# Kernel tuning notes

Hardware: AMD Instinct MI355X
Metric: run time of the kernel (lower is better)

Reference implementation:

```python
import jax, jax.numpy as jnp
import numpy as np

SEQ_LEN = 512
DIM = 256
HEADS = 8
DIM_HEAD = 32
INNER = HEADS * DIM_HEAD
BATCH = 1
LN_EPS = 1e-5


def setup_inputs() -> dict:
    key = jax.random.key(0)
    ks = jax.random.split(key, 6)
    # kaiming_uniform_(a=sqrt(5)) on [L, in, out] -> bound = 1/sqrt(fan_in) with fan_in = in_dim*out_dim? 
    # torch computes fan_in from dims [1:] => fan_in = in_dim (dim of -2) * ... in practice bound ~ sqrt(1/fan_in);
    # exact init distribution is irrelevant for correctness testing, use uniform(+-1/sqrt(DIM)).
    s = 1.0 / np.sqrt(DIM)
    so = 1.0 / np.sqrt(INNER)
    return {
        "x": jax.random.normal(ks[0], (BATCH, SEQ_LEN, DIM), jnp.float32),
        "Wq": jax.random.uniform(ks[1], (SEQ_LEN, DIM, INNER), jnp.float32, -s, s),
        "Wk": jax.random.uniform(ks[2], (SEQ_LEN, DIM, INNER), jnp.float32, -s, s),
        "Wv": jax.random.uniform(ks[3], (SEQ_LEN, DIM, INNER), jnp.float32, -s, s),
        "gamma": jnp.ones((DIM,), jnp.float32),
        "beta": jnp.zeros((DIM,), jnp.float32),
        "Wo": jax.random.uniform(ks[4], (INNER, DIM), jnp.float32, -so, so),
        "bo": jnp.zeros((DIM,), jnp.float32),
    }


def reference(x, Wq, Wk, Wv, gamma, beta, Wo, bo):
    b, n, dim = x.shape
    h, dh = HEADS, DIM_HEAD
    # LayerNorm
    mu = jnp.mean(x, axis=-1, keepdims=True)
    var = jnp.mean((x - mu) ** 2, axis=-1, keepdims=True)
    xn = (x - mu) / jnp.sqrt(var + LN_EPS) * gamma + beta
    # Per-relative-index projections: pd[b, r, m, e] = xn[b, m] @ W[r]
    qd = jnp.einsum('bmc,rce->brme', xn, Wq)
    kd = jnp.einsum('bmc,rce->brme', xn, Wk)
    vd = jnp.einsum('bmc,rce->brme', xn, Wv)
    i = jnp.arange(n)
    # to_q / to_v index map: max(0, i - j); to_k (after rearrange swap) uses min(0, m - n) + n - 1
    rq = jnp.maximum(0, i[:, None] - i[None, :])          # [n(query), m(key)]
    rk = jnp.minimum(0, i[None, :] - i[:, None]) + n - 1  # [n, m]
    # q[b,n,m,e] = qd[b, rq[n,m], m]; k[b,n,m,e] = kd[b, rk[n,m], n]; v like q
    q_full = qd[:, rq, i[None, :], :].reshape(b, n, n, h, dh)
    k_full = kd[:, rk, i[:, None], :].reshape(b, n, n, h, dh)
    v_full = vd[:, rq, i[None, :], :].reshape(b, n, n, h, dh)
    scale = dh ** -0.5
    dots = jnp.einsum('bnmhd,bnmhd->bhnm', q_full, k_full) * scale
    causal = i[:, None] >= i[None, :]  # tril
    dots = jnp.where(causal[None, None], dots, -jnp.inf)
    attn = jax.nn.softmax(dots, axis=-1)
    out = jnp.einsum('bhnm,bnmhd->bnhd', attn, v_full).reshape(b, n, h * dh)
    return out @ Wo + bo
```

## Files before the change

kernel.cpp:

```cpp
#include <hip/hip_runtime.h>
#include <hip/hip_bf16.h>

typedef unsigned short u16;
typedef unsigned int   u32;
typedef __bf16 bf16x8 __attribute__((ext_vector_type(8)));
typedef float  f32x4  __attribute__((ext_vector_type(4)));
typedef u32    u32x4  __attribute__((ext_vector_type(4)));
typedef u32    u32x2  __attribute__((ext_vector_type(2)));

#define TRI_TOTAL 131328

__device__ __forceinline__ float b2f(u16 u) {
    return __builtin_bit_cast(float, ((u32)u) << 16);
}
__device__ __forceinline__ u16 f2b(float f) {
    u32 u = __builtin_bit_cast(u32, f);
    return (u16)((u + 0x7fffu + ((u >> 16) & 1u)) >> 16);
}

__global__ void __launch_bounds__(256) ln_kernel(const float* __restrict__ x,
                                                 const float* __restrict__ g,
                                                 const float* __restrict__ b,
                                                 u16* __restrict__ xn) {
    int n = blockIdx.x, t = threadIdx.x;
    float v = x[n * 256 + t];
    __shared__ float red[4];
    float s = v;
    #pragma unroll
    for (int o = 32; o >= 1; o >>= 1) s += __shfl_xor(s, o);
    if ((t & 63) == 0) red[t >> 6] = s;
    __syncthreads();
    float mu = (red[0] + red[1] + red[2] + red[3]) * (1.0f / 256.0f);
    float d = v - mu;
    __syncthreads();
    float s2 = d * d;
    #pragma unroll
    for (int o = 32; o >= 1; o >>= 1) s2 += __shfl_xor(s2, o);
    if ((t & 63) == 0) red[t >> 6] = s2;
    __syncthreads();
    float var = (red[0] + red[1] + red[2] + red[3]) * (1.0f / 256.0f);
    float y = d * rsqrtf(var + 1e-5f) * g[t] + b[t];
    xn[n * 256 + t] = f2b(y);
}

__global__ void __launch_bounds__(256) proj_kernel(
        const u16* __restrict__ xn,
        const float* __restrict__ Wq, const float* __restrict__ Wk,
        const float* __restrict__ Wv,
        u16* __restrict__ Qa, u16* __restrict__ Ka, u16* __restrict__ Va) {
    __shared__ u16 Wl[64 * 256];
    __shared__ u16 Al[64 * 256];

    int bid = blockIdx.x;
    int which = bid >> 11;
    int rr = bid & 2047;
    int r  = (which == 1) ? (511 - (rr >> 2)) : (rr >> 2);
    int cs = rr & 3;
    const float* W = (which == 0) ? Wq : ((which == 1) ? Wk : Wv);
    u16* Out       = (which == 0) ? Qa : ((which == 1) ? Ka : Va);
    int rows  = (which == 1) ? (r + 1) : (512 - r);
    int pbase = (which == 1) ? (511 - r) : 0;
    int nbase = (which == 1) ? (511 - r) : r;

    int t = threadIdx.x;
    int c0 = cs * 64;

    int srow   = t >> 5;
    int slot16 = (t & 31) * 16;
    char* adp = (char*)Al + srow * 512 + (slot16 ^ (srow << 4));
    u32x4 ar0, ar1, ar2, ar3, ar4, ar5, ar6, ar7;

#define A_LOAD(M0) do {                                                       \
    int gg;                                                                   \
    gg = pbase + (M0) +  0 + srow; if (gg > 511) gg = 511;                    \
    ar0 = *(const u32x4*)((const char*)xn + (size_t)gg * 512 + slot16);       \
    gg = pbase + (M0) +  8 + srow; if (gg > 511) gg = 511;                    \
    ar1 = *(const u32x4*)((const char*)xn + (size_t)gg * 512 + slot16);       \
    gg = pbase + (M0) + 16 + srow; if (gg > 511) gg = 511;                    \
    ar2 = *(const u32x4*)((const char*)xn + (size_t)gg * 512 + slot16);       \
    gg = pbase + (M0) + 24 + srow; if (gg > 511) gg = 511;                    \
    ar3 = *(const u32x4*)((const char*)xn + (size_t)gg * 512 + slot16);       \
    gg = pbase + (M0) + 32 + srow; if (gg > 511) gg = 511;                    \
    ar4 = *(const u32x4*)((const char*)xn + (size_t)gg * 512 + slot16);       \
    gg = pbase + (M0) + 40 + srow; if (gg > 511) gg = 511;                    \
    ar5 = *(const u32x4*)((const char*)xn + (size_t)gg * 512 + slot16);       \
    gg = pbase + (M0) + 48 + srow; if (gg > 511) gg = 511;                    \
    ar6 = *(const u32x4*)((const char*)xn + (size_t)gg * 512 + slot16);       \
    gg = pbase + (M0) + 56 + srow; if (gg > 511) gg = 511;                    \
    ar7 = *(const u32x4*)((const char*)xn + (size_t)gg * 512 + slot16);       \
} while (0)

#define A_WRITE() do {                                                        \
    *(u32x4*)(adp + 0 * 4096) = ar0;                                          \
    *(u32x4*)(adp + 1 * 4096) = ar1;                                          \
    *(u32x4*)(adp + 2 * 4096) = ar2;                                          \
    *(u32x4*)(adp + 3 * 4096) = ar3;                                          \
    *(u32x4*)(adp + 4 * 4096) = ar4;                                          \
    *(u32x4*)(adp + 5 * 4096) = ar5;                                          \
    *(u32x4*)(adp + 6 * 4096) = ar6;                                          \
    *(u32x4*)(adp + 7 * 4096) = ar7;                                          \
} while (0)

    {
        int c4 = (t & 15) * 4;
        int kq = t >> 4;
        const float* wp = W + ((size_t)r << 16) + c0 + c4 + (size_t)(kq * 4) * 256;
        f32x4 w00 = *(const f32x4*)(wp + 0 * 256);
        f32x4 w01 = *(const f32x4*)(wp + 1 * 256);
        f32x4 w02 = *(const f32x4*)(wp + 2 * 256);
        f32x4 w03 = *(const f32x4*)(wp + 3 * 256);
        f32x4 w10 = *(const f32x4*)(wp + 16384 + 0 * 256);
        f32x4 w11 = *(const f32x4*)(wp + 16384 + 1 * 256);
        f32x4 w12 = *(const f32x4*)(wp + 16384 + 2 * 256);
        f32x4 w13 = *(const f32x4*)(wp + 16384 + 3 * 256);
        f32x4 w20 = *(const f32x4*)(wp + 32768 + 0 * 256);
        f32x4 w21 = *(const f32x4*)(wp + 32768 + 1 * 256);
        f32x4 w22 = *(const f32x4*)(wp + 32768 + 2 * 256);
        f32x4 w23 = *(const f32x4*)(wp + 32768 + 3 * 256);
        f32x4 w30 = *(const f32x4*)(wp + 49152 + 0 * 256);
        f32x4 w31 = *(const f32x4*)(wp + 49152 + 1 * 256);
        f32x4 w32 = *(const f32x4*)(wp + 49152 + 2 * 256);
        f32x4 w33 = *(const f32x4*)(wp + 49152 + 3 * 256);
        A_LOAD(0);
#define WLW(IT, VA, VB, VC, VD) {                                             \
        int kbase = kq * 4 + (IT) * 64;                                       \
        _Pragma("unroll")                                                     \
        for (int i = 0; i < 4; ++i) {                                         \
            int col = c4 + i;                                                 \
            u32 lo = (u32)f2b(VA[i]) | ((u32)f2b(VB[i]) << 16);               \
            u32 hi = (u32)f2b(VC[i]) | ((u32)f2b(VD[i]) << 16);               \
            u32x2 pr; pr[0] = lo; pr[1] = hi;                                 \
            *(u32x2*)((char*)Wl + col * 512 +                                 \
                      ((kbase * 2) ^ ((col & 31) << 4))) = pr;                \
        }                                                                     \
    }
        WLW(0, w00, w01, w02, w03)
        WLW(1, w10, w11, w12, w13)
        WLW(2, w20, w21, w22, w23)
        WLW(3, w30, w31, w32, w33)
#undef WLW
    }
    __syncthreads();

    int wv  = t >> 6;
    int L   = t & 63;
    int l15 = L & 15, l4 = L >> 4;
    int rbase = wv * 16;
    const char* wb = (const char*)Wl;
    const char* al_row = (const char*)Al + (rbase + l15) * 512;
    int amask = ((rbase + l15) & 7) << 4;
    int cA = l15, cB = 16 + l15, cC = 32 + l15, cD = 48 + l15;
    int swA = (cA & 31) << 4, swB = (cB & 31) << 4;
    int swC = (cC & 31) << 4, swD = (cD & 31) << 4;

    for (int m0 = 0; m0 < rows; m0 += 64) {
        A_WRITE();
        __syncthreads();
        if (m0 + 64 < rows) A_LOAD(m0 + 64);

        f32x4 acc0 = {}, acc1 = {}, acc2 = {}, acc3 = {};
#define KS(ks) {                                                              \
        int kb = (ks) * 64 + l4 * 16;                                         \
        bf16x8 a  = *(const bf16x8*)(al_row + (kb ^ amask));                  \
        bf16x8 b0 = *(const bf16x8*)(wb + cA * 512 + (kb ^ swA));             \
        bf16x8 b1 = *(const bf16x8*)(wb + cB * 512 + (kb ^ swB));             \
        bf16x8 b2 = *(const bf16x8*)(wb + cC * 512 + (kb ^ swC));             \
        bf16x8 b3 = *(const bf16x8*)(wb + cD * 512 + (kb ^ swD));             \
        acc0 = __builtin_amdgcn_mfma_f32_16x16x32_bf16(a, b0, acc0, 0, 0, 0); \
        acc1 = __builtin_amdgcn_mfma_f32_16x16x32_bf16(a, b1, acc1, 0, 0, 0); \
        acc2 = __builtin_amdgcn_mfma_f32_16x16x32_bf16(a, b2, acc2, 0, 0, 0); \
        acc3 = __builtin_amdgcn_mfma_f32_16x16x32_bf16(a, b3, acc3, 0, 0, 0); \
    }
        KS(0) KS(1) KS(2) KS(3) KS(4) KS(5) KS(6) KS(7)
#undef KS

        #pragma unroll
        for (int j = 0; j < 4; ++j) {
            int ml = m0 + rbase + l4 * 4 + j;
            if (ml < rows) {
                int nout = nbase + ml;
                size_t prow = (size_t)(nout * (nout + 1) / 2) + (size_t)ml;
                u16* op = Out + prow * 256 + c0 + l15;
                op[0]  = f2b(acc0[j]);
                op[16] = f2b(acc1[j]);
                op[32] = f2b(acc2[j]);
                op[48] = f2b(acc3[j]);
            }
        }
        __syncthreads();
    }
#undef A_LOAD
#undef A_WRITE
}

__global__ void __launch_bounds__(256) attn_kernel(const u16* __restrict__ Qa,
                                                   const u16* __restrict__ Ka,
                                                   const u16* __restrict__ Va,
                                                   float* __restrict__ ao) {
    int n = blockIdx.x, t = threadIdx.x;
    __shared__ float pbuf[512 * 9];
    __shared__ float linv[8];
    int band = n + 1;
    size_t rb = (size_t)(n * (n + 1) / 2);

    int h = t & 7, mi = t >> 3;
    for (int m0 = 0; m0 < band; m0 += 32) {
        int m = m0 + mi;
        float d = -1e30f;
        if (m < band) {
            const char* qp = (const char*)Qa + (rb + m) * 512 + h * 64;
            const char* kp = (const char*)Ka + (rb + m) * 512 + h * 64;
            float acc = 0.f;
            #pragma unroll
            for (int cch = 0; cch < 4; ++cch) {
                u32x4 qv = *reinterpret_cast<const u32x4*>(qp + cch * 16);
                u32x4 kv = *reinterpret_cast<const u32x4*>(kp + cch * 16);
                #pragma unroll
                for (int i = 0; i < 4; ++i) {
                    float ql = __builtin_bit_cast(float, qv[i] << 16);
                    float qh = __builtin_bit_cast(float, qv[i] & 0xffff0000u);
                    float kl = __builtin_bit_cast(float, kv[i] << 16);
                    float kh = __builtin_bit_cast(float, kv[i] & 0xffff0000u);
                    acc += ql * kl + qh * kh;
                }
            }
            d = acc * 0.17677669529663687f;
        }
        pbuf[m * 9 + h] = d;
    }
    __syncthreads();

    int wv = t >> 6, L = t & 63;
    for (int s = 0; s < 2; ++s) {
        int hh = wv + s * 4;
        float mx = -1e30f;
        for (int m = L; m < band; m += 64) mx = fmaxf(mx, pbuf[m * 9 + hh]);
        #pragma unroll
        for (int o = 32; o >= 1; o >>= 1) mx = fmaxf(mx, __shfl_xor(mx, o));
        float sum = 0.f;
        for (int m = L; m < band; m += 64) {
            float p = __expf(pbuf[m * 9 + hh] - mx);
            pbuf[m * 9 + hh] = p;
            sum += p;
        }
        #pragma unroll
        for (int o = 32; o >= 1; o >>= 1) sum += __shfl_xor(sum, o);
        if (L == 0) linv[hh] = 1.0f / sum;
    }
    __syncthreads();

    int h2 = t >> 5;
    const char* vp = (const char*)Va + rb * 512 + (size_t)t * 2;
    const float* pb = pbuf + h2;
    float a0 = 0, a1 = 0, a2 = 0, a3 = 0;
    int m = 0;
    for (; m + 4 <= band; m += 4) {
        a0 += pb[(m + 0) * 9] * b2f(*(const u16*)(vp + (size_t)(m + 0) * 512));
        a1 += pb[(m + 1) * 9] * b2f(*(const u16*)(vp + (size_t)(m + 1) * 512));
        a2 += pb[(m + 2) * 9] * b2f(*(const u16*)(vp + (size_t)(m + 2) * 512));
        a3 += pb[(m + 3) * 9] * b2f(*(const u16*)(vp + (size_t)(m + 3) * 512));
    }
    for (; m < band; ++m)
        a0 += pb[m * 9] * b2f(*(const u16*)(vp + (size_t)m * 512));
    ao[n * 256 + t] = ((a0 + a1) + (a2 + a3)) * linv[h2];
}

__global__ void __launch_bounds__(256) outproj_kernel(const float* __restrict__ ao,
                                                      const float* __restrict__ Wo,
                                                      const float* __restrict__ bo,
                                                      float* __restrict__ out) {
    int n = blockIdx.x, e = threadIdx.x;
    const float* a = ao + n * 256;
    float c0 = bo[e], c1 = 0, c2 = 0, c3 = 0;
    for (int c = 0; c < 256; c += 4) {
        c0 += a[c + 0] * Wo[(c + 0) * 256 + e];
        c1 += a[c + 1] * Wo[(c + 1) * 256 + e];
        c2 += a[c + 2] * Wo[(c + 2) * 256 + e];
        c3 += a[c + 3] * Wo[(c + 3) * 256 + e];
    }
    out[n * 256 + e] = (c0 + c1) + (c2 + c3);
}

extern "C" void kernel_launch(void* const* d_in, const int* in_sizes, int n_in,
                              void* d_out, int out_size, void* d_ws, size_t ws_size,
                              hipStream_t stream) {
    const float* x     = (const float*)d_in[0];
    const float* Wq    = (const float*)d_in[1];
    const float* Wk    = (const float*)d_in[2];
    const float* Wv    = (const float*)d_in[3];
    const float* gamma = (const float*)d_in[4];
    const float* beta  = (const float*)d_in[5];
    const float* Wo    = (const float*)d_in[6];
    const float* bo    = (const float*)d_in[7];
    float* out = (float*)d_out;

    char* ws = (char*)d_ws;
    u16* xn = (u16*)ws;
    size_t off = (size_t)512 * 256 * 2;
    u16* Qa = (u16*)(ws + off); off += (size_t)TRI_TOTAL * 256 * 2;
    u16* Ka = (u16*)(ws + off); off += (size_t)TRI_TOTAL * 256 * 2;
    u16* Va = (u16*)(ws + off); off += (size_t)TRI_TOTAL * 256 * 2;
    float* ao = (float*)(ws + off);

    ln_kernel<<<512, 256, 0, stream>>>(x, gamma, beta, xn);
    proj_kernel<<<6144, 256, 0, stream>>>(xn, Wq, Wk, Wv, Qa, Ka, Va);
    attn_kernel<<<512, 256, 0, stream>>>(Qa, Ka, Va, ao);
    outproj_kernel<<<512, 256, 0, stream>>>(ao, Wo, bo, out);
}
```

Measured before the change: 274.0 us.

## Split projection tile across eight waves with column-group partitioning

Doubles the projection kernel block to 512 threads. The 64x64 output tile is now split into 4 row groups and 2 column groups, so each wave computes 16x32 instead of 16x64. Weight and activation staging loads are spread over twice as many threads, with fewer registers held per thread, and the LDS swizzle for weight columns changes to a new XOR pattern. The aim is more memory-level parallelism and latency hiding on the bandwidth-heavy weight reads, at the cost of per-wave fragment reuse and larger blocks that may limit how many blocks fit per CU.

```diff
diff --git a/kernel.cpp b/kernel.cpp
--- a/kernel.cpp
+++ b/kernel.cpp
@@ -16,6 +16,9 @@
 __device__ __forceinline__ u16 f2b(float f) {
     u32 u = __builtin_bit_cast(u32, f);
     return (u16)((u + 0x7fffu + ((u >> 16) & 1u)) >> 16);
+}
+__device__ __forceinline__ int pcol(int col) {
+    return (((col & 7) ^ ((col >> 3) & 7)) << 4);
 }
 
 __global__ void __launch_bounds__(256) ln_kernel(const float* __restrict__ x,
@@ -43,7 +46,7 @@
     xn[n * 256 + t] = f2b(y);
 }
 
-__global__ void __launch_bounds__(256) proj_kernel(
+__global__ void __launch_bounds__(512) proj_kernel(
         const u16* __restrict__ xn,
         const float* __restrict__ Wq, const float* __restrict__ Wk,
         const float* __restrict__ Wv,
@@ -67,109 +70,82 @@
 
     int srow   = t >> 5;
     int slot16 = (t & 31) * 16;
-    char* adp = (char*)Al + srow * 512 + (slot16 ^ (srow << 4));
-    u32x4 ar0, ar1, ar2, ar3, ar4, ar5, ar6, ar7;
+    char* adp = (char*)Al + srow * 512 + (slot16 ^ ((srow & 7) << 4));
+    u32x4 ar0, ar1, ar2, ar3;
 
 #define A_LOAD(M0) do {                                                       \
     int gg;                                                                   \
     gg = pbase + (M0) +  0 + srow; if (gg > 511) gg = 511;                    \
     ar0 = *(const u32x4*)((const char*)xn + (size_t)gg * 512 + slot16);       \
-    gg = pbase + (M0) +  8 + srow; if (gg > 511) gg = 511;                    \
+    gg = pbase + (M0) + 16 + srow; if (gg > 511) gg = 511;                    \
     ar1 = *(const u32x4*)((const char*)xn + (size_t)gg * 512 + slot16);       \
-    gg = pbase + (M0) + 16 + srow; if (gg > 511) gg = 511;                    \
+    gg = pbase + (M0) + 32 + srow; if (gg > 511) gg = 511;                    \
     ar2 = *(const u32x4*)((const char*)xn + (size_t)gg * 512 + slot16);       \
-    gg = pbase + (M0) + 24 + srow; if (gg > 511) gg = 511;                    \
+    gg = pbase + (M0) + 48 + srow; if (gg > 511) gg = 511;                    \
     ar3 = *(const u32x4*)((const char*)xn + (size_t)gg * 512 + slot16);       \
-    gg = pbase + (M0) + 32 + srow; if (gg > 511) gg = 511;                    \
-    ar4 = *(const u32x4*)((const char*)xn + (size_t)gg * 512 + slot16);       \
-    gg = pbase + (M0) + 40 + srow; if (gg > 511) gg = 511;                    \
-    ar5 = *(const u32x4*)((const char*)xn + (size_t)gg * 512 + slot16);       \
-    gg = pbase + (M0) + 48 + srow; if (gg > 511) gg = 511;                    \
-    ar6 = *(const u32x4*)((const char*)xn + (size_t)gg * 512 + slot16);       \
-    gg = pbase + (M0) + 56 + srow; if (gg > 511) gg = 511;                    \
-    ar7 = *(const u32x4*)((const char*)xn + (size_t)gg * 512 + slot16);       \
 } while (0)
 
 #define A_WRITE() do {                                                        \
-    *(u32x4*)(adp + 0 * 4096) = ar0;                                          \
-    *(u32x4*)(adp + 1 * 4096) = ar1;                                          \
-    *(u32x4*)(adp + 2 * 4096) = ar2;                                          \
-    *(u32x4*)(adp + 3 * 4096) = ar3;                                          \
-    *(u32x4*)(adp + 4 * 4096) = ar4;                                          \
-    *(u32x4*)(adp + 5 * 4096) = ar5;                                          \
-    *(u32x4*)(adp + 6 * 4096) = ar6;                                          \
-    *(u32x4*)(adp + 7 * 4096) = ar7;                                          \
+    *(u32x4*)(adp + 0 * 8192) = ar0;                                          \
+    *(u32x4*)(adp + 1 * 8192) = ar1;                                          \
+    *(u32x4*)(adp + 2 * 8192) = ar2;                                          \
+    *(u32x4*)(adp + 3 * 8192) = ar3;                                          \
 } while (0)
 
     {
         int c4 = (t & 15) * 4;
         int kq = t >> 4;
         const float* wp = W + ((size_t)r << 16) + c0 + c4 + (size_t)(kq * 4) * 256;
-        f32x4 w00 = *(const f32x4*)(wp + 0 * 256);
-        f32x4 w01 = *(const f32x4*)(wp + 1 * 256);
-        f32x4 w02 = *(const f32x4*)(wp + 2 * 256);
-        f32x4 w03 = *(const f32x4*)(wp + 3 * 256);
-        f32x4 w10 = *(const f32x4*)(wp + 16384 + 0 * 256);
-        f32x4 w11 = *(const f32x4*)(wp + 16384 + 1 * 256);
-        f32x4 w12 = *(const f32x4*)(wp + 16384 + 2 * 256);
-        f32x4 w13 = *(const f32x4*)(wp + 16384 + 3 * 256);
-        f32x4 w20 = *(const f32x4*)(wp + 32768 + 0 * 256);
-        f32x4 w21 = *(const f32x4*)(wp + 32768 + 1 * 256);
-        f32x4 w22 = *(const f32x4*)(wp + 32768 + 2 * 256);
-        f32x4 w23 = *(const f32x4*)(wp + 32768 + 3 * 256);
-        f32x4 w30 = *(const f32x4*)(wp + 49152 + 0 * 256);
-        f32x4 w31 = *(const f32x4*)(wp + 49152 + 1 * 256);
-        f32x4 w32 = *(const f32x4*)(wp + 49152 + 2 * 256);
-        f32x4 w33 = *(const f32x4*)(wp + 49152 + 3 * 256);
+        f32x4 w00 = *(const f32x4*)(wp + 0);
+        f32x4 w01 = *(const f32x4*)(wp + 256);
+        f32x4 w02 = *(const f32x4*)(wp + 512);
+        f32x4 w03 = *(const f32x4*)(wp + 768);
+        f32x4 w10 = *(const f32x4*)(wp + 32768 + 0);
+        f32x4 w11 = *(const f32x4*)(wp + 32768 + 256);
+        f32x4 w12 = *(const f32x4*)(wp + 32768 + 512);
+        f32x4 w13 = *(const f32x4*)(wp + 32768 + 768);
         A_LOAD(0);
 #define WLW(IT, VA, VB, VC, VD) {                                             \
-        int kbase = kq * 4 + (IT) * 64;                                       \
+        int kbase2 = (kq * 4 + (IT) * 128) * 2;                               \
         _Pragma("unroll")                                                     \
         for (int i = 0; i < 4; ++i) {                                         \
             int col = c4 + i;                                                 \
             u32 lo = (u32)f2b(VA[i]) | ((u32)f2b(VB[i]) << 16);               \
             u32 hi = (u32)f2b(VC[i]) | ((u32)f2b(VD[i]) << 16);               \
             u32x2 pr; pr[0] = lo; pr[1] = hi;                                 \
-            *(u32x2*)((char*)Wl + col * 512 +                                 \
-                      ((kbase * 2) ^ ((col & 31) << 4))) = pr;                \
+            *(u32x2*)((char*)Wl + col * 512 + (kbase2 ^ pcol(col))) = pr;     \
         }                                                                     \
     }
         WLW(0, w00, w01, w02, w03)
         WLW(1, w10, w11, w12, w13)
-        WLW(2, w20, w21, w22, w23)
-        WLW(3, w30, w31, w32, w33)
 #undef WLW
     }
-    __syncthreads();
 
     int wv  = t >> 6;
+    int mg  = wv & 3;
+    int cg  = wv >> 2;
     int L   = t & 63;
     int l15 = L & 15, l4 = L >> 4;
-    int rbase = wv * 16;
+    int rbase = mg * 16;
     const char* wb = (const char*)Wl;
     const char* al_row = (const char*)Al + (rbase + l15) * 512;
     int amask = ((rbase + l15) & 7) << 4;
-    int cA = l15, cB = 16 + l15, cC = 32 + l15, cD = 48 + l15;
-    int swA = (cA & 31) << 4, swB = (cB & 31) << 4;
-    int swC = (cC & 31) << 4, swD = (cD & 31) << 4;
+    int cA = cg * 32 + l15, cB = cg * 32 + 16 + l15;
+    int swA = pcol(cA), swB = pcol(cB);
 
     for (int m0 = 0; m0 < rows; m0 += 64) {
         A_WRITE();
         __syncthreads();
         if (m0 + 64 < rows) A_LOAD(m0 + 64);
 
-        f32x4 acc0 = {}, acc1 = {}, acc2 = {}, acc3 = {};
+        f32x4 acc0 = {}, acc1 = {};
 #define KS(ks) {                                                              \
         int kb = (ks) * 64 + l4 * 16;                                         \
         bf16x8 a  = *(const bf16x8*)(al_row + (kb ^ amask));                  \
         bf16x8 b0 = *(const bf16x8*)(wb + cA * 512 + (kb ^ swA));             \
         bf16x8 b1 = *(const bf16x8*)(wb + cB * 512 + (kb ^ swB));             \
-        bf16x8 b2 = *(const bf16x8*)(wb + cC * 512 + (kb ^ swC));             \
-        bf16x8 b3 = *(const bf16x8*)(wb + cD * 512 + (kb ^ swD));             \
         acc0 = __builtin_amdgcn_mfma_f32_16x16x32_bf16(a, b0, acc0, 0, 0, 0); \
         acc1 = __builtin_amdgcn_mfma_f32_16x16x32_bf16(a, b1, acc1, 0, 0, 0); \
-        acc2 = __builtin_amdgcn_mfma_f32_16x16x32_bf16(a, b2, acc2, 0, 0, 0); \
-        acc3 = __builtin_amdgcn_mfma_f32_16x16x32_bf16(a, b3, acc3, 0, 0, 0); \
     }
         KS(0) KS(1) KS(2) KS(3) KS(4) KS(5) KS(6) KS(7)
 #undef KS
@@ -180,11 +156,9 @@
             if (ml < rows) {
                 int nout = nbase + ml;
                 size_t prow = (size_t)(nout * (nout + 1) / 2) + (size_t)ml;
-                u16* op = Out + prow * 256 + c0 + l15;
+                u16* op = Out + prow * 256 + c0 + cg * 32 + l15;
                 op[0]  = f2b(acc0[j]);
                 op[16] = f2b(acc1[j]);
-                op[32] = f2b(acc2[j]);
-                op[48] = f2b(acc3[j]);
             }
         }
         __syncthreads();
@@ -303,7 +277,7 @@
     float* ao = (float*)(ws + off);
 
     ln_kernel<<<512, 256, 0, stream>>>(x, gamma, beta, xn);
-    proj_kernel<<<6144, 256, 0, stream>>>(xn, Wq, Wk, Wv, Qa, Ka, Va);
+    proj_kernel<<<6144, 512, 0, stream>>>(xn, Wq, Wk, Wv, Qa, Ka, Va);
     attn_kernel<<<512, 256, 0, stream>>>(Qa, Ka, Va, ao);
     outproj_kernel<<<512, 256, 0, stream>>>(ao, Wo, bo, out);
 }
```

New measurement: 278.9 us. About the same (+1.8%).
